# Kernel tuning notes

Hardware: AMD Instinct MI355X
Metric: run time of the kernel (lower is better)

The kernel has to match this reference:

```python
import jax, jax.numpy as jnp
import numpy as np

N, E, VD, HD, ES = 10000, 80000, 32, 64, 68
NET_IN = VD * VD + 2 * HD + ES   # 1220: f2s(1024) + s[e0](64) + s[e1](64) + edge_s(68)
SELF_IN = VD * VD + 2 * HD       # 1152: temp_f2s(1024) + s(64) + s_c(64)
OUT_D = VD * VD + HD             # 1088: vector channel mixer + scalar update


def _lecun(k, fin, fout):
    return jax.random.normal(k, (fin, fout), jnp.float32) / jnp.sqrt(jnp.float32(fin))


def setup_inputs() -> dict:
    ks = jax.random.split(jax.random.key(0), 16)
    return {
        "f": jax.random.normal(ks[0], (N, 3, VD), jnp.float32),
        "s": jax.random.normal(ks[1], (N, HD), jnp.float32),
        "edge_f": jax.random.normal(ks[2], (E, 3, 1), jnp.float32),
        "edge_s": jax.random.normal(ks[3], (E, ES), jnp.float32),
        "W_emb1": _lecun(ks[4], 2 * VD + 1, VD),
        "net_W1": _lecun(ks[5], NET_IN, HD), "net_b1": jnp.zeros((HD,), jnp.float32),
        "net_W2": _lecun(ks[6], HD, HD), "net_b2": jnp.zeros((HD,), jnp.float32),
        "net_W3": _lecun(ks[7], HD, OUT_D), "net_b3": jnp.zeros((OUT_D,), jnp.float32),
        "W_emb2": _lecun(ks[8], 2 * VD, VD),
        "self_W1": _lecun(ks[9], SELF_IN, HD), "self_b1": jnp.zeros((HD,), jnp.float32),
        "self_W2": _lecun(ks[10], HD, HD), "self_b2": jnp.zeros((HD,), jnp.float32),
        "self_W3": _lecun(ks[11], HD, OUT_D), "self_b3": jnp.zeros((OUT_D,), jnp.float32),
        "edge_index": jax.random.randint(ks[12], (2, E), 0, N),
    }


def _mlp(x, W1, b1, W2, b2, W3, b3):
    h = jax.nn.relu(x @ W1 + b1)
    h = jax.nn.relu(h @ W2 + b2)
    return h @ W3 + b3


def _segment_mean(x, ids, n):
    tot = jax.ops.segment_sum(x, ids, num_segments=n)
    cnt = jax.ops.segment_sum(jnp.ones(ids.shape, x.dtype), ids, num_segments=n)
    return tot / jnp.maximum(cnt, 1.0).reshape((n,) + (1,) * (x.ndim - 1))


def _forward(f, s, edge_f, edge_s,
             W_emb1, net_W1, net_b1, net_W2, net_b2, net_W3, net_b3,
             W_emb2, self_W1, self_b1, self_W2, self_b2, self_W3, self_b3,
             edge_index):
    n = f.shape[0]
    e0, e1 = edge_index[0], edge_index[1]
    # --- edge message: gather -> embed -> gram einsum -> MLP ---
    _f = jnp.concatenate((f[e0], f[e1], edge_f), axis=-1)          # [E,3,2VD+1]
    _s = jnp.concatenate((s[e0], s[e1], edge_s), axis=-1)          # [E,2HD+ES]
    _f = _f @ W_emb1                                               # [E,3,VD]
    f2s = jnp.einsum('eij,eik->ejk', _f, _f).reshape(-1, VD * VD)  # _f^T @ _f, [E,VD*VD]
    Fn = jnp.linalg.norm(f2s, axis=-1, keepdims=True) + 1.0
    c = _mlp(jnp.concatenate((f2s, _s), axis=-1),
             net_W1, net_b1, net_W2, net_b2, net_W3, net_b3) / Fn  # [E,OUT_D]
    f_c = jnp.einsum('eij,ejk->eik', _f, c[:, :VD * VD].reshape(-1, VD, VD))  # [E,3,VD]
    f_c = _segment_mean(f_c, e0, n)                                # [N,3,VD]
    s_c = _segment_mean(c[:, VD * VD:], e0, n)                     # [N,HD]
    # --- node self-update ---
    tf = jnp.concatenate((f, f_c), axis=-1) @ W_emb2               # [N,3,VD]
    tf2s = jnp.einsum('nij,nik->njk', tf, tf).reshape(n, VD * VD)
    Fn2 = jnp.linalg.norm(tf2s, axis=-1, keepdims=True) + 1.0
    c2 = _mlp(jnp.concatenate((tf2s, s, s_c), axis=-1),
              self_W1, self_b1, self_W2, self_b2, self_W3, self_b3) / Fn2
    f_out = jnp.einsum('nij,njk->nik', tf, c2[:, :VD * VD].reshape(-1, VD, VD)) + f
    s_out = c2[:, VD * VD:] + s
    return f_out, s_out


def reference(f, s, edge_f, edge_s,
              W_emb1, net_W1, net_b1, net_W2, net_b2, net_W3, net_b3,
              W_emb2, self_W1, self_b1, self_W2, self_b2, self_W3, self_b3,
              edge_index):
    return _forward(f, s, edge_f, edge_s,
                    W_emb1, net_W1, net_b1, net_W2, net_b2, net_W3, net_b3,
                    W_emb2, self_W1, self_b1, self_W2, self_b2, self_W3, self_b3,
                    edge_index)
```

## Files before the change

### kernel.cpp

```cpp
#include <hip/hip_runtime.h>
#include <math.h>

#define NN 10000
#define NE 80000
#define SFH 102
#define SFB 98
#define SSB 66
#define STX 72
#define NTRI 528
#define SAE 104
#define SAN 72

typedef __attribute__((ext_vector_type(8))) __bf16 bf16x8;
typedef __attribute__((ext_vector_type(8))) short short8v;
typedef __attribute__((ext_vector_type(4))) float f32x4;
typedef __attribute__((ext_vector_type(4))) unsigned uint4v;

__device__ __forceinline__ ushort f2bf(float x) {
  union { float f; unsigned u; } v; v.f = x;
  unsigned r = v.u + 0x7FFFu + ((v.u >> 16) & 1u);
  return (ushort)(r >> 16);
}
__device__ __forceinline__ float bfu(ushort u) {
  union { unsigned x; float f; } v; v.x = (unsigned)u << 16;
  return v.f;
}
__device__ __forceinline__ void tri_ab(int k, int& a, int& b) {
  int aa = 0, rem = k;
  while (rem >= 32 - aa) { rem -= 32 - aa; ++aa; }
  a = aa; b = aa + rem;
}

__global__ __launch_bounds__(1024)
void sgnn_scan(const int* __restrict__ deg, int* __restrict__ cursor,
               int* __restrict__ start) {
  __shared__ int sm[1024];
  __shared__ int carry;
  const int t = threadIdx.x;
  if (t == 0) carry = 0;
  __syncthreads();
  for (int base = 0; base < NN; base += 1024) {
    const int i = base + t;
    const int v = (i < NN) ? deg[i] : 0;
    sm[t] = v;
    __syncthreads();
    #pragma unroll
    for (int d = 1; d < 1024; d <<= 1) {
      const int add = (t >= d) ? sm[t - d] : 0;
      __syncthreads();
      sm[t] += add;
      __syncthreads();
    }
    const int excl = carry + sm[t] - v;
    if (i < NN) { cursor[i] = excl; start[i] = excl; }
    __syncthreads();
    if (t == 1023) carry += sm[1023];
    __syncthreads();
  }
}

__global__ __launch_bounds__(256)
void sgnn_scatter(const int* __restrict__ eidx, int* __restrict__ cursor,
                  int* __restrict__ sorted) {
  const int e = blockIdx.x * 256 + threadIdx.x;
  if (e < NE) {
    const int p = atomicAdd(cursor + eidx[e], 1);
    sorted[p] = e;
  }
}

__global__ __launch_bounds__(256)
void sgnn_wconv(const float* __restrict__ nW1, const float* __restrict__ nW2,
                const float* __restrict__ nW3, const float* __restrict__ sW1,
                const float* __restrict__ sW2, const float* __restrict__ sW3,
                const float* __restrict__ Wemb1, const float* __restrict__ Wemb2,
                const int* __restrict__ eidx, int* __restrict__ deg,
                ushort* __restrict__ wout, ushort* __restrict__ tab) {
  const int gid = blockIdx.x * 256 + threadIdx.x;
  if (gid < NE) atomicAdd(deg + eidx[gid], 1);
  if (gid >= 61 * 4096) {
    const int k = gid - 61 * 4096;
    if (k < NTRI) {
      int a, b; tri_ab(k, a, b);
      tab[k] = (ushort)(a | (b << 8) | ((a != b) ? 0x8000 : 0));
    }
    return;
  }
  const int tile = gid >> 12, idx = gid & 4095;
  const int c = idx >> 6, k = idx & 63;
  float v = 0.f;
  if (tile < 12) {
    const int T = tile;
    if (T < 8 || (T == 8 && k < 16)) {
      const int ktri = T * 64 + k;
      if (ktri < NTRI) {
        int a, b; tri_ab(ktri, a, b);
        v = nW1[(a * 32 + b) * 64 + c];
        if (a != b) v += nW1[(b * 32 + a) * 64 + c];
      }
    } else if (T == 8) { if (k < 20) v = nW1[(1216 + (k - 16)) * 64 + c]; }
    else if (T == 9)   v = nW1[(1024 + k) * 64 + c];
    else if (T == 10)  v = nW1[(1088 + k) * 64 + c];
    else               v = nW1[(1152 + k) * 64 + c];
  } else if (tile == 12) v = nW2[k * 64 + c];
  else if (tile < 30)    v = nW3[k * 1088 + (tile - 13) * 64 + c];
  else if (tile < 41) {
    const int T = tile - 30;
    if (T < 8 || (T == 8 && k < 16)) {
      const int ktri = T * 64 + k;
      if (ktri < NTRI) {
        int a, b; tri_ab(ktri, a, b);
        v = sW1[(a * 32 + b) * 64 + c];
        if (a != b) v += sW1[(b * 32 + a) * 64 + c];
      }
    } else if (T == 9) v = sW1[(1024 + k) * 64 + c];
    else if (T == 10)  v = sW1[(1088 + k) * 64 + c];
  } else if (tile == 41) v = sW2[k * 64 + c];
  else if (tile < 59)    v = sW3[k * 1088 + (tile - 42) * 64 + c];
  else if (tile == 59) {
    const int col = idx / 96, kk = idx % 96;
    v = (col < 32 && kk < 65) ? Wemb1[kk * 32 + col] : 0.f;
  } else {
    const int col = idx >> 6;
    v = (col < 32) ? Wemb2[k * 32 + col] : 0.f;
  }
  wout[gid] = f2bf(v);
}

#define STAGE_W(srcbase) do { const ushort* _s = (srcbase);                      \
  _Pragma("unroll") for (int rr = 0; rr < 2; ++rr) {                             \
    const int idx_ = t + 256 * rr; const int c_ = idx_ >> 3, ko_ = idx_ & 7;     \
    *(short8v*)&Wl[c_ * STX + ko_ * 8] = *(const short8v*)&_s[c_ * 64 + ko_ * 8];\
  } } while (0)

#define WPRE_LOAD(srcbase) do { const ushort* _s = (srcbase);                    \
  wpre0 = *(const short8v*)&_s[(t >> 3) * 64 + (t & 7) * 8];                     \
  wpre1 = *(const short8v*)&_s[(32 + (t >> 3)) * 64 + (t & 7) * 8]; } while (0)

#define WPRE_STORE() do {                                                        \
  *(short8v*)&Wl[(t >> 3) * STX + (t & 7) * 8] = wpre0;                          \
  *(short8v*)&Wl[(32 + (t >> 3)) * STX + (t & 7) * 8] = wpre1; } while (0)

#define MFMA_K64() do {                                                          \
  _Pragma("unroll") for (int kb = 0; kb < 2; ++kb) {                             \
    const bf16x8 af_ = *(const bf16x8*)&Xl[(w * 16 + ll) * STX + kb * 32 + lh * 8]; \
    acc[0] = __builtin_amdgcn_mfma_f32_16x16x32_bf16(af_,                        \
        *(const bf16x8*)&Wl[(     ll) * STX + kb * 32 + lh * 8], acc[0], 0, 0, 0); \
    acc[1] = __builtin_amdgcn_mfma_f32_16x16x32_bf16(af_,                        \
        *(const bf16x8*)&Wl[(16 + ll) * STX + kb * 32 + lh * 8], acc[1], 0, 0, 0); \
    acc[2] = __builtin_amdgcn_mfma_f32_16x16x32_bf16(af_,                        \
        *(const bf16x8*)&Wl[(32 + ll) * STX + kb * 32 + lh * 8], acc[2], 0, 0, 0); \
    acc[3] = __builtin_amdgcn_mfma_f32_16x16x32_bf16(af_,                        \
        *(const bf16x8*)&Wl[(48 + ll) * STX + kb * 32 + lh * 8], acc[3], 0, 0, 0); \
  } } while (0)

#define ZERO_ACC() do { _Pragma("unroll") for (int q = 0; q < 4; ++q)            \
    acc[q] = (f32x4){0.f, 0.f, 0.f, 0.f}; } while (0)

#define PACK_STORE16(dstp) do {                                                  \
  unsigned pk[8];                                                                \
  _Pragma("unroll") for (int q = 0; q < 8; ++q)                                  \
    pk[q] = (unsigned)f2bf(xv[2 * q]) | ((unsigned)f2bf(xv[2 * q + 1]) << 16);   \
  *(uint4v*)(dstp)       = (uint4v){pk[0], pk[1], pk[2], pk[3]};                 \
  *(uint4v*)((dstp) + 8) = (uint4v){pk[4], pk[5], pk[6], pk[7]};                 \
} while (0)

#define TRI16(kt) do {                                                           \
  int prev_a = -1; float fa0 = 0.f, fa1 = 0.f, fa2 = 0.f;                        \
  _Pragma("unroll") for (int m = 0; m < 16; ++m) {                               \
    const int tb = tabL[(kt) + m];                                               \
    const int a_ = tb & 31, b_ = (tb >> 8) & 31;                                 \
    if (a_ != prev_a) { fa0 = bfu(fr[a_]); fa1 = bfu(fr[32 + a_]);               \
                        fa2 = bfu(fr[64 + a_]); prev_a = a_; }                   \
    const float v = fmaf(fa0, bfu(fr[b_]),                                       \
        fmaf(fa1, bfu(fr[32 + b_]), fa2 * bfu(fr[64 + b_])));                    \
    const float wsel = (tb & 0x8000) ? 2.f : 1.f;                                \
    sumsq = fmaf(v * wsel, v, sumsq);                                            \
    xv[m] = v;                                                                   \
  } } while (0)

#define XV_LOAD16(p) do { const float* _p = (p);                                 \
  _Pragma("unroll") for (int q = 0; q < 4; ++q) {                                \
    const float4 v4 = *(const float4*)(_p + 4 * q);                              \
    xv[4 * q + 0] = v4.x; xv[4 * q + 1] = v4.y;                                  \
    xv[4 * q + 2] = v4.z; xv[4 * q + 3] = v4.w; } } while (0)

#define CONSUME_NT() do {                                                        \
  _Pragma("unroll") for (int r = 0; r < 4; ++r) {                                \
    const int row_ = w * 16 + lh * 4 + r;                                        \
    const unsigned u0 = *(const unsigned*)&smFh[row_ * SFH +      nt * 2];       \
    const unsigned u1 = *(const unsigned*)&smFh[row_ * SFH + 32 + nt * 2];       \
    const unsigned u2 = *(const unsigned*)&smFh[row_ * SFH + 64 + nt * 2];       \
    union { unsigned x; float f; } l0, h0, l1, h1, l2, h2;                       \
    l0.x = u0 << 16; h0.x = u0 & 0xffff0000u;                                    \
    l1.x = u1 << 16; h1.x = u1 & 0xffff0000u;                                    \
    l2.x = u2 << 16; h2.x = u2 & 0xffff0000u;                                    \
    _Pragma("unroll") for (int nc = 0; nc < 4; ++nc) {                           \
      const float cv = (acc[nc][r] + b3v[nc]) * ifnr[r];                         \
      const int p = nc & 1;                                                      \
      const float f0 = (nc < 2) ? l0.f : h0.f;                                   \
      const float f1 = (nc < 2) ? l1.f : h1.f;                                   \
      const float f2 = (nc < 2) ? l2.f : h2.f;                                   \
      fch[(r * 3 + 0) * 2 + p] = fmaf(f0, cv, fch[(r * 3 + 0) * 2 + p]);         \
      fch[(r * 3 + 1) * 2 + p] = fmaf(f1, cv, fch[(r * 3 + 1) * 2 + p]);         \
      fch[(r * 3 + 2) * 2 + p] = fmaf(f2, cv, fch[(r * 3 + 2) * 2 + p]);         \
    }                                                                            \
  } } while (0)

#define STAGE_FS() do {                                                          \
  _Pragma("unroll") for (int r = 0; r < 4; ++r) {                                \
    const int row_ = w * 16 + lh * 4 + r;                                        \
    _Pragma("unroll") for (int i = 0; i < 3; ++i) {                              \
      F[row_ * SFB + i * 32 + ll]      = f2bf(fch[(r * 3 + i) * 2 + 0]);         \
      F[row_ * SFB + i * 32 + ll + 16] = f2bf(fch[(r * 3 + i) * 2 + 1]);         \
    }                                                                            \
    _Pragma("unroll") for (int nc = 0; nc < 4; ++nc)                             \
      S[row_ * SSB + nc * 16 + ll] = f2bf(cs[nc * 4 + r]);                       \
  } } while (0)

#define LDS_BYTES 34656

__global__ __launch_bounds__(256, 2)
void sgnn_edge(const float* __restrict__ f, const float* __restrict__ s,
               const float* __restrict__ edge_f, const float* __restrict__ edge_s,
               const float* __restrict__ b1, const float* __restrict__ b2,
               const float* __restrict__ b3,
               const ushort* __restrict__ wbf, const ushort* __restrict__ tab_g,
               const int* __restrict__ eidx, const int* __restrict__ sorted,
               const int* __restrict__ start_g, const int* __restrict__ deg_g,
               float* __restrict__ fc_sum, float* __restrict__ sc_sum) {
  __shared__ __align__(16) char sbuf[LDS_BYTES];
  ushort* smFh = (ushort*)sbuf;
  ushort* F    = (ushort*)sbuf;
  ushort* Xl   = (ushort*)(sbuf + 13056);
  ushort* S    = (ushort*)(sbuf + 13056);
  ushort* Aemb = (ushort*)(sbuf + 13056);
  ushort* Wl   = (ushort*)(sbuf + 22272);
  float*  red  = (float*)(sbuf + 31488);
  int*    snode = (int*)(sbuf + 31488);
  int*    srow0 = snode + 8;
  int*    srow1 = snode + 16;
  int*    sst   = snode + 24;
  int*    sdg   = snode + 32;
  ushort* tabL = (ushort*)(sbuf + 33088);
  float*  iFn  = (float*)(sbuf + 33088);
  int*    es_s = (int*)(sbuf + 34144);
  ushort* e0s  = (ushort*)(sbuf + 34400);
  ushort* e1s  = (ushort*)(sbuf + 34528);

  const int t = threadIdx.x, j = t & 63, w = t >> 6, eb = w * 16;
  const int lh = j >> 4, ll = j & 15;
  const int bid = blockIdx.x;
  const ushort* wembT = wbf + 59 * 4096;
  short8v wpre0, wpre1;

  if (t < 64) {
    const int e = sorted[bid * 64 + t];
    es_s[t] = e;
    e0s[t] = (ushort)eidx[e];
    e1s[t] = (ushort)eidx[NE + e];
  }
  for (int idx = t; idx < NTRI; idx += 256) tabL[idx] = tab_g[idx];
  __syncthreads();

  int str = 0, dgr = 0;
  if (j < 16) {
    const int n_ = e0s[eb + j];
    str = start_g[n_];
    dgr = deg_g[n_];
  }
  WPRE_LOAD(wbf + 0);

  #pragma unroll 1
  for (int h = 0; h < 2; ++h) {
    const int hb = h * 32;
    #pragma unroll 1
    for (int cc = t; cc < 576; cc += 256) {
      const int row = cc / 6, seg = cc - row * 6;
      const int lel = (row * 43) >> 7, il = row - lel * 3;
      const int k0 = seg * 16;
      float xv[16];
      if (seg < 4) {
        const int nd = (seg < 2) ? (int)e0s[hb + lel] : (int)e1s[hb + lel];
        XV_LOAD16(f + nd * 96 + il * 32 + (seg & 1) * 16);
      } else if (seg == 4) {
        xv[0] = edge_f[es_s[hb + lel] * 3 + il];
        #pragma unroll
        for (int m = 1; m < 16; ++m) xv[m] = 0.f;
      } else {
        #pragma unroll
        for (int m = 0; m < 16; ++m) xv[m] = 0.f;
      }
      PACK_STORE16(&Aemb[row * SAE + k0]);
    }
    __syncthreads();
    #pragma unroll 1
    for (int job = w * 3; job < w * 3 + 3; ++job) {
      const int mt = job >> 1, nt = job & 1;
      f32x4 ac = (f32x4){0.f, 0.f, 0.f, 0.f};
      #pragma unroll
      for (int kb = 0; kb < 3; ++kb) {
        const bf16x8 av = *(const bf16x8*)&Aemb[(mt * 16 + ll) * SAE + kb * 32 + lh * 8];
        const bf16x8 bv = *(const bf16x8*)&wembT[(nt * 16 + ll) * 96 + kb * 32 + lh * 8];
        ac = __builtin_amdgcn_mfma_f32_16x16x32_bf16(av, bv, ac, 0, 0, 0);
      }
      #pragma unroll
      for (int r = 0; r < 4; ++r) {
        const int rr = mt * 16 + lh * 4 + r;
        const int lel = (rr * 43) >> 7, il = rr - lel * 3;
        smFh[(hb + lel) * SFH + il * 32 + nt * 16 + ll] = f2bf(ac[r]);
      }
    }
    __syncthreads();
  }

  f32x4 acc[4];
  ZERO_ACC();
  float sumsq = 0.f;

  #pragma unroll 1
  for (int T = 0; T < 12; ++T) {
    __syncthreads();
    WPRE_STORE();
    {
      const ushort* fr = smFh + j * SFH;
      float xv[16];
      if (T < 8) {
        TRI16(T * 64 + w * 16);
      } else if (T == 8) {
        if (w == 0) {
          TRI16(512);
        } else if (w == 1) {
          const float4 v4 = *(const float4*)(edge_s + es_s[j] * 68 + 64);
          xv[0] = v4.x; xv[1] = v4.y; xv[2] = v4.z; xv[3] = v4.w;
          #pragma unroll
          for (int m = 4; m < 16; ++m) xv[m] = 0.f;
        } else {
          #pragma unroll
          for (int m = 0; m < 16; ++m) xv[m] = 0.f;
        }
      } else if (T == 9)  { XV_LOAD16(s + e0s[j] * 64 + w * 16); }
      else if (T == 10)   { XV_LOAD16(s + e1s[j] * 64 + w * 16); }
      else                { XV_LOAD16(edge_s + es_s[j] * 68 + w * 16); }
      PACK_STORE16(&Xl[j * STX + w * 16]);
    }
    __syncthreads();
    WPRE_LOAD(wbf + (T + 1) * 4096);
    MFMA_K64();
  }

  __syncthreads();
  red[w * 64 + j] = sumsq;
  #pragma unroll
  for (int nc = 0; nc < 4; ++nc) {
    const float bv = b1[nc * 16 + ll];
    #pragma unroll
    for (int r = 0; r < 4; ++r)
      Xl[(w * 16 + lh * 4 + r) * STX + nc * 16 + ll] = f2bf(fmaxf(acc[nc][r] + bv, 0.f));
  }
  WPRE_STORE();
  ZERO_ACC();
  __syncthreads();
  if (t < 64) {
    const float ss = red[t] + red[64 + t] + red[128 + t] + red[192 + t];
    iFn[t] = 1.f / (sqrtf(ss) + 1.f);
  }

  MFMA_K64();
  #pragma unroll
  for (int nc = 0; nc < 4; ++nc) {
    const float bv = b2[nc * 16 + ll];
    #pragma unroll
    for (int r = 0; r < 4; ++r)
      Xl[(w * 16 + lh * 4 + r) * STX + nc * 16 + ll] = f2bf(fmaxf(acc[nc][r] + bv, 0.f));
  }

  float fch[24];
  #pragma unroll
  for (int q = 0; q < 24; ++q) fch[q] = 0.f;
  float cs[16];
  float ifnr[4];

  #pragma unroll 1
  for (int nt = 0; nt < 17; ++nt) {
    __syncthreads();
    STAGE_W(wbf + (13 + nt) * 4096);
    float b3v[4];
    #pragma unroll
    for (int nc = 0; nc < 4; ++nc) b3v[nc] = b3[nt * 64 + nc * 16 + ll];
    __syncthreads();
    if (nt == 0) {
      #pragma unroll
      for (int r = 0; r < 4; ++r) ifnr[r] = iFn[w * 16 + lh * 4 + r];
    }
    ZERO_ACC();
    MFMA_K64();
    if (nt < 16) {
      CONSUME_NT();
    } else {
      #pragma unroll
      for (int nc = 0; nc < 4; ++nc)
        #pragma unroll
        for (int r = 0; r < 4; ++r)
          cs[nc * 4 + r] = (acc[nc][r] + b3v[nc]) * ifnr[r];
    }
  }

  __syncthreads();
  STAGE_FS();
  if (t < 8) snode[t] = -1;
  __syncthreads();

  {
    float r0 = 0.f, r1 = 0.f, rs = 0.f;
    int runlen = 0;
    const int gwb = bid * 64 + eb;
    #pragma unroll 1
    for (int m = 0; m < 16; ++m) {
      const int row = eb + m;
      r0 += bfu(F[row * SFB + j]);
      if (j < 32) r1 += bfu(F[row * SFB + 64 + j]);
      rs += bfu(S[row * SSB + j]);
      ++runlen;
      const int n = e0s[row];
      if (m == 15 || e0s[row + 1] != n) {
        const int st = __shfl(str, m);
        const int dg = __shfl(dgr, m);
        const int g1v = gwb + m, g0v = g1v - runlen + 1;
        if (g0v == st && runlen == dg) {
          fc_sum[n * 96 + j] = r0;
          if (j < 32) fc_sum[n * 96 + 64 + j] = r1;
          sc_sum[n * 64 + j] = rs;
        } else {
          const int slot = (g0v == gwb) ? 2 * w : 2 * w + 1;
          if (j == 0) {
            snode[slot] = n; srow0[slot] = row - runlen + 1; srow1[slot] = row;
            sst[slot] = st; sdg[slot] = dg;
          }
        }
        r0 = r1 = rs = 0.f; runlen = 0;
      }
    }
  }
  __syncthreads();

  if (t < 160) {
    const int ch = t;
    int prevn = -1;
    #pragma unroll 1
    for (int ss = 0; ss < 8; ++ss) {
      const int n = snode[ss];
      if (n < 0) continue;
      if (n != prevn) {
        float v = 0.f;
        #pragma unroll 1
        for (int k2 = ss; k2 < 8; ++k2) {
          if (snode[k2] == n) {
            #pragma unroll 1
            for (int row = srow0[k2]; row <= srow1[k2]; ++row)
              v += (ch < 96) ? bfu(F[row * SFB + ch]) : bfu(S[row * SSB + (ch - 96)]);
          } else if (k2 > ss && snode[k2] >= 0) break;
        }
        const bool cib = (sst[ss] >= bid * 64) && (sst[ss] + sdg[ss] <= bid * 64 + 64);
        float* dst = (ch < 96) ? (fc_sum + n * 96 + ch) : (sc_sum + n * 64 + (ch - 96));
        if (cib) *dst = v; else atomicAdd(dst, v);
      }
      prevn = n;
    }
  }
}

__global__ __launch_bounds__(256, 2)
void sgnn_node(const float* __restrict__ f, const float* __restrict__ s,
               const float* __restrict__ b1, const float* __restrict__ b2,
               const float* __restrict__ b3,
               const ushort* __restrict__ wbf, const ushort* __restrict__ tab_g,
               const float* __restrict__ fcm, const float* __restrict__ scm,
               const int* __restrict__ deg_g,
               float* __restrict__ of, float* __restrict__ os) {
  __shared__ __align__(16) char sbuf[LDS_BYTES];
  ushort* smFh = (ushort*)sbuf;
  ushort* F    = (ushort*)sbuf;
  ushort* Xl   = (ushort*)(sbuf + 13056);
  ushort* S    = (ushort*)(sbuf + 13056);
  ushort* Aemb = (ushort*)(sbuf + 13056);
  ushort* Wl   = (ushort*)(sbuf + 22272);
  float*  red  = (float*)(sbuf + 31488);
  float*  icntL = (float*)(sbuf + 31488);
  ushort* tabL = (ushort*)(sbuf + 33088);
  float*  iFn  = (float*)(sbuf + 33088);

  const int t = threadIdx.x, j = t & 63, w = t >> 6, eb = w * 16;
  const int lh = j >> 4, ll = j & 15;
  const int nbase = blockIdx.x * 64;
  const ushort* wembTn = wbf + 60 * 4096;
  short8v wpre0, wpre1;

  for (int idx = t; idx < NTRI; idx += 256) tabL[idx] = tab_g[idx];
  if (t < 64)
    icntL[t] = 1.f / fmaxf((float)deg_g[min(nbase + t, NN - 1)], 1.f);
  WPRE_LOAD(wbf + 30 * 4096);
  __syncthreads();

  #pragma unroll 1
  for (int h = 0; h < 2; ++h) {
    const int hb = h * 32;
    #pragma unroll 1
    for (int cc = t; cc < 384; cc += 256) {
      const int row = cc >> 2, seg = cc & 3;
      const int lel = (row * 43) >> 7, il = row - lel * 3;
      const int nc = min(nbase + hb + lel, NN - 1);
      const int k0 = seg * 16;
      float xv[16];
      if (seg < 2) {
        XV_LOAD16(f + nc * 96 + il * 32 + seg * 16);
      } else {
        XV_LOAD16(fcm + nc * 96 + il * 32 + (seg - 2) * 16);
        const float ic = icntL[hb + lel];
        #pragma unroll
        for (int m = 0; m < 16; ++m) xv[m] *= ic;
      }
      PACK_STORE16(&Aemb[row * SAN + k0]);
    }
    __syncthreads();
    #pragma unroll 1
    for (int job = w * 3; job < w * 3 + 3; ++job) {
      const int mt = job >> 1, nt = job & 1;
      f32x4 ac = (f32x4){0.f, 0.f, 0.f, 0.f};
      #pragma unroll
      for (int kb = 0; kb < 2; ++kb) {
        const bf16x8 av = *(const bf16x8*)&Aemb[(mt * 16 + ll) * SAN + kb * 32 + lh * 8];
        const bf16x8 bv = *(const bf16x8*)&wembTn[(nt * 16 + ll) * 64 + kb * 32 + lh * 8];
        ac = __builtin_amdgcn_mfma_f32_16x16x32_bf16(av, bv, ac, 0, 0, 0);
      }
      #pragma unroll
      for (int r = 0; r < 4; ++r) {
        const int rr = mt * 16 + lh * 4 + r;
        const int lel = (rr * 43) >> 7, il = rr - lel * 3;
        smFh[(hb + lel) * SFH + il * 32 + nt * 16 + ll] = f2bf(ac[r]);
      }
    }
    __syncthreads();
  }

  f32x4 acc[4];
  ZERO_ACC();
  float sumsq = 0.f;

  #pragma unroll 1
  for (int T = 0; T < 11; ++T) {
    __syncthreads();
    WPRE_STORE();
    {
      const ushort* fr = smFh + j * SFH;
      float xv[16];
      if (T < 8) {
        TRI16(T * 64 + w * 16);
      } else if (T == 8) {
        if (w == 0) {
          TRI16(512);
        } else {
          #pragma unroll
          for (int m = 0; m < 16; ++m) xv[m] = 0.f;
        }
      } else if (T == 9) {
        XV_LOAD16(s + min(nbase + j, NN - 1) * 64 + w * 16);
      } else {
        XV_LOAD16(scm + min(nbase + j, NN - 1) * 64 + w * 16);
        const float ic = icntL[j];
        #pragma unroll
        for (int m = 0; m < 16; ++m) xv[m] *= ic;
      }
      PACK_STORE16(&Xl[j * STX + w * 16]);
    }
    __syncthreads();
    WPRE_LOAD(wbf + (31 + T) * 4096);
    MFMA_K64();
  }

  __syncthreads();
  red[w * 64 + j] = sumsq;
  #pragma unroll
  for (int nc = 0; nc < 4; ++nc) {
    const float bv = b1[nc * 16 + ll];
    #pragma unroll
    for (int r = 0; r < 4; ++r)
      Xl[(w * 16 + lh * 4 + r) * STX + nc * 16 + ll] = f2bf(fmaxf(acc[nc][r] + bv, 0.f));
  }
  WPRE_STORE();
  ZERO_ACC();
  __syncthreads();
  if (t < 64) {
    const float ss = red[t] + red[64 + t] + red[128 + t] + red[192 + t];
    iFn[t] = 1.f / (sqrtf(ss) + 1.f);
  }

  MFMA_K64();
  #pragma unroll
  for (int nc = 0; nc < 4; ++nc) {
    const float bv = b2[nc * 16 + ll];
    #pragma unroll
    for (int r = 0; r < 4; ++r)
      Xl[(w * 16 + lh * 4 + r) * STX + nc * 16 + ll] = f2bf(fmaxf(acc[nc][r] + bv, 0.f));
  }

  float fch[24];
  #pragma unroll
  for (int q = 0; q < 24; ++q) fch[q] = 0.f;
  float cs[16];
  float ifnr[4];

  #pragma unroll 1
  for (int nt = 0; nt < 17; ++nt) {
    __syncthreads();
    STAGE_W(wbf + (42 + nt) * 4096);
    float b3v[4];
    #pragma unroll
    for (int nc = 0; nc < 4; ++nc) b3v[nc] = b3[nt * 64 + nc * 16 + ll];
    __syncthreads();
    if (nt == 0) {
      #pragma unroll
      for (int r = 0; r < 4; ++r) ifnr[r] = iFn[w * 16 + lh * 4 + r];
    }
    ZERO_ACC();
    MFMA_K64();
    if (nt < 16) {
      CONSUME_NT();
    } else {
      #pragma unroll
      for (int nc = 0; nc < 4; ++nc)
        #pragma unroll
        for (int r = 0; r < 4; ++r)
          cs[nc * 4 + r] = (acc[nc][r] + b3v[nc]) * ifnr[r];
    }
  }

  __syncthreads();
  STAGE_FS();
  __syncthreads();

  #pragma unroll 1
  for (int m = 0; m < 16; ++m) {
    const int row = eb + m;
    const int n_m = nbase + row;
    if (n_m < NN) {
      of[n_m * 96 + j] = bfu(F[row * SFB + j]) + f[n_m * 96 + j];
      if (j < 32)
        of[n_m * 96 + 64 + j] = bfu(F[row * SFB + 64 + j]) + f[n_m * 96 + 64 + j];
      os[n_m * 64 + j] = bfu(S[row * SSB + j]) + s[n_m * 64 + j];
    }
  }
}

extern "C" void kernel_launch(void* const* d_in, const int* in_sizes, int n_in,
                              void* d_out, int out_size, void* d_ws, size_t ws_size,
                              hipStream_t stream) {
  const float* f      = (const float*)d_in[0];
  const float* s      = (const float*)d_in[1];
  const float* edge_f = (const float*)d_in[2];
  const float* edge_s = (const float*)d_in[3];
  const float* Wemb1  = (const float*)d_in[4];
  const float* nW1 = (const float*)d_in[5];
  const float* nb1 = (const float*)d_in[6];
  const float* nW2 = (const float*)d_in[7];
  const float* nb2 = (const float*)d_in[8];
  const float* nW3 = (const float*)d_in[9];
  const float* nb3 = (const float*)d_in[10];
  const float* Wemb2 = (const float*)d_in[11];
  const float* sW1 = (const float*)d_in[12];
  const float* sb1 = (const float*)d_in[13];
  const float* sW2 = (const float*)d_in[14];
  const float* sb2 = (const float*)d_in[15];
  const float* sW3 = (const float*)d_in[16];
  const float* sb3 = (const float*)d_in[17];
  const int* eidx  = (const int*)d_in[18];

  float* of = (float*)d_out;
  float* os = of + (size_t)NN * 96;

  int* deg    = (int*)d_ws;
  int* cursor = deg + NN;
  int* start  = cursor + NN;
  int* sorted = start + NN;
  ushort* wbf = (ushort*)(sorted + NE);
  ushort* tab = wbf + 61 * 4096;

  hipMemsetAsync(deg, 0, (size_t)NN * 4, stream);
  hipMemsetAsync(d_out, 0, (size_t)NN * 160 * 4, stream);

  hipLaunchKernelGGL(sgnn_wconv, dim3((61 * 4096 + NTRI + 255) / 256), dim3(256),
                     0, stream, nW1, nW2, nW3, sW1, sW2, sW3, Wemb1, Wemb2,
                     eidx, deg, wbf, tab);
  hipLaunchKernelGGL(sgnn_scan, dim3(1), dim3(1024), 0, stream, deg, cursor, start);
  hipLaunchKernelGGL(sgnn_scatter, dim3((NE + 255) / 256), dim3(256), 0, stream,
                     eidx, cursor, sorted);
  hipLaunchKernelGGL(sgnn_edge, dim3(NE / 64), dim3(256), 0, stream,
                     f, s, edge_f, edge_s, nb1, nb2, nb3,
                     wbf, tab, eidx, sorted, start, deg,
                     of , os );
  hipLaunchKernelGGL(sgnn_node, dim3((NN + 63) / 64), dim3(256), 0, stream,
                     f, s, sb1, sb2, sb3,
                     wbf, tab, of , os , deg, of, os);
}
```

Before: 213.2 us.

## Double-buffer X and W LDS tiles to overlap staging with MFMA

Adds a second LDS buffer for both the activation tile and the weight tile in the edge and node kernels. The next K-tile's features are built and its weights stored while the current tile's MFMAs run, so each loop step needs one barrier instead of two. The W3 loop also switches from synchronous staging to register-prefetched, double-buffered weights. LDS per block grows from about 34.6KB to 52.5KB, which may limit how many blocks fit per CU at the requested two blocks.

Result: slower. 236.2 us (+10.8%).

```diff
diff --git a/kernel.cpp b/kernel.cpp
--- a/kernel.cpp
+++ b/kernel.cpp
@@ -127,31 +127,25 @@
   wout[gid] = f2bf(v);
 }
 
-#define STAGE_W(srcbase) do { const ushort* _s = (srcbase);                      \
-  _Pragma("unroll") for (int rr = 0; rr < 2; ++rr) {                             \
-    const int idx_ = t + 256 * rr; const int c_ = idx_ >> 3, ko_ = idx_ & 7;     \
-    *(short8v*)&Wl[c_ * STX + ko_ * 8] = *(const short8v*)&_s[c_ * 64 + ko_ * 8];\
-  } } while (0)
-
 #define WPRE_LOAD(srcbase) do { const ushort* _s = (srcbase);                    \
   wpre0 = *(const short8v*)&_s[(t >> 3) * 64 + (t & 7) * 8];                     \
   wpre1 = *(const short8v*)&_s[(32 + (t >> 3)) * 64 + (t & 7) * 8]; } while (0)
 
-#define WPRE_STORE() do {                                                        \
-  *(short8v*)&Wl[(t >> 3) * STX + (t & 7) * 8] = wpre0;                          \
-  *(short8v*)&Wl[(32 + (t >> 3)) * STX + (t & 7) * 8] = wpre1; } while (0)
-
-#define MFMA_K64() do {                                                          \
+#define WPRE_STORE_TO(Wd) do { ushort* _d = (Wd);                                \
+  *(short8v*)&_d[(t >> 3) * STX + (t & 7) * 8] = wpre0;                          \
+  *(short8v*)&_d[(32 + (t >> 3)) * STX + (t & 7) * 8] = wpre1; } while (0)
+
+#define MFMA_K64_B(Xb, Wb) do { const ushort* _x = (Xb); const ushort* _wl = (Wb);\
   _Pragma("unroll") for (int kb = 0; kb < 2; ++kb) {                             \
-    const bf16x8 af_ = *(const bf16x8*)&Xl[(w * 16 + ll) * STX + kb * 32 + lh * 8]; \
+    const bf16x8 af_ = *(const bf16x8*)&_x[(w * 16 + ll) * STX + kb * 32 + lh * 8]; \
     acc[0] = __builtin_amdgcn_mfma_f32_16x16x32_bf16(af_,                        \
-        *(const bf16x8*)&Wl[(     ll) * STX + kb * 32 + lh * 8], acc[0], 0, 0, 0); \
+        *(const bf16x8*)&_wl[(     ll) * STX + kb * 32 + lh * 8], acc[0], 0, 0, 0); \
     acc[1] = __builtin_amdgcn_mfma_f32_16x16x32_bf16(af_,                        \
-        *(const bf16x8*)&Wl[(16 + ll) * STX + kb * 32 + lh * 8], acc[1], 0, 0, 0); \
+        *(const bf16x8*)&_wl[(16 + ll) * STX + kb * 32 + lh * 8], acc[1], 0, 0, 0); \
     acc[2] = __builtin_amdgcn_mfma_f32_16x16x32_bf16(af_,                        \
-        *(const bf16x8*)&Wl[(32 + ll) * STX + kb * 32 + lh * 8], acc[2], 0, 0, 0); \
+        *(const bf16x8*)&_wl[(32 + ll) * STX + kb * 32 + lh * 8], acc[2], 0, 0, 0); \
     acc[3] = __builtin_amdgcn_mfma_f32_16x16x32_bf16(af_,                        \
-        *(const bf16x8*)&Wl[(48 + ll) * STX + kb * 32 + lh * 8], acc[3], 0, 0, 0); \
+        *(const bf16x8*)&_wl[(48 + ll) * STX + kb * 32 + lh * 8], acc[3], 0, 0, 0); \
   } } while (0)
 
 #define ZERO_ACC() do { _Pragma("unroll") for (int q = 0; q < 4; ++q)            \
@@ -218,7 +212,7 @@
       S[row_ * SSB + nc * 16 + ll] = f2bf(cs[nc * 4 + r]);                       \
   } } while (0)
 
-#define LDS_BYTES 34656
+#define LDS_BYTES 52512
 
 __global__ __launch_bounds__(256, 2)
 void sgnn_edge(const float* __restrict__ f, const float* __restrict__ s,
@@ -232,21 +226,23 @@
   __shared__ __align__(16) char sbuf[LDS_BYTES];
   ushort* smFh = (ushort*)sbuf;
   ushort* F    = (ushort*)sbuf;
-  ushort* Xl   = (ushort*)(sbuf + 13056);
+  ushort* Xl0  = (ushort*)(sbuf + 13056);
   ushort* S    = (ushort*)(sbuf + 13056);
   ushort* Aemb = (ushort*)(sbuf + 13056);
-  ushort* Wl   = (ushort*)(sbuf + 22272);
-  float*  red  = (float*)(sbuf + 31488);
-  int*    snode = (int*)(sbuf + 31488);
+  ushort* Xl1  = (ushort*)(sbuf + 22272);
+  ushort* Wl0  = (ushort*)(sbuf + 31488);
+  ushort* Wl1  = (ushort*)(sbuf + 40704);
+  float*  red  = (float*)(sbuf + 49920);
+  int*    snode = (int*)(sbuf + 49920);
   int*    srow0 = snode + 8;
   int*    srow1 = snode + 16;
   int*    sst   = snode + 24;
   int*    sdg   = snode + 32;
-  ushort* tabL = (ushort*)(sbuf + 33088);
-  float*  iFn  = (float*)(sbuf + 33088);
-  int*    es_s = (int*)(sbuf + 34144);
-  ushort* e0s  = (ushort*)(sbuf + 34400);
-  ushort* e1s  = (ushort*)(sbuf + 34528);
+  ushort* tabL = (ushort*)(sbuf + 50944);
+  float*  iFn  = (float*)(sbuf + 50944);
+  int*    es_s = (int*)(sbuf + 52000);
+  ushort* e0s  = (ushort*)(sbuf + 52256);
+  ushort* e1s  = (ushort*)(sbuf + 52384);
 
   const int t = threadIdx.x, j = t & 63, w = t >> 6, eb = w * 16;
   const int lh = j >> 4, ll = j & 15;
@@ -318,47 +314,53 @@
   ZERO_ACC();
   float sumsq = 0.f;
 
+  #define XSTAGE_E(T, Xd) do { ushort* _xd = (Xd);                               \
+    const ushort* fr = smFh + j * SFH;                                           \
+    float xv[16];                                                                \
+    if ((T) < 8) { TRI16((T) * 64 + w * 16); }                                   \
+    else if ((T) == 8) {                                                         \
+      if (w == 0) { TRI16(512); }                                                \
+      else if (w == 1) {                                                         \
+        const float4 v4 = *(const float4*)(edge_s + es_s[j] * 68 + 64);          \
+        xv[0] = v4.x; xv[1] = v4.y; xv[2] = v4.z; xv[3] = v4.w;                  \
+        _Pragma("unroll") for (int m = 4; m < 16; ++m) xv[m] = 0.f;              \
+      } else { _Pragma("unroll") for (int m = 0; m < 16; ++m) xv[m] = 0.f; }     \
+    }                                                                            \
+    else if ((T) == 9)  { XV_LOAD16(s + e0s[j] * 64 + w * 16); }                 \
+    else if ((T) == 10) { XV_LOAD16(s + e1s[j] * 64 + w * 16); }                 \
+    else                { XV_LOAD16(edge_s + es_s[j] * 68 + w * 16); }           \
+    PACK_STORE16(&_xd[j * STX + w * 16]);                                        \
+  } while (0)
+
+  XSTAGE_E(0, Xl0);
+  WPRE_STORE_TO(Wl0);
+  WPRE_LOAD(wbf + 1 * 4096);
+  __syncthreads();
   #pragma unroll 1
   for (int T = 0; T < 12; ++T) {
-    __syncthreads();
-    WPRE_STORE();
-    {
-      const ushort* fr = smFh + j * SFH;
-      float xv[16];
-      if (T < 8) {
-        TRI16(T * 64 + w * 16);
-      } else if (T == 8) {
-        if (w == 0) {
-          TRI16(512);
-        } else if (w == 1) {
-          const float4 v4 = *(const float4*)(edge_s + es_s[j] * 68 + 64);
-          xv[0] = v4.x; xv[1] = v4.y; xv[2] = v4.z; xv[3] = v4.w;
-          #pragma unroll
-          for (int m = 4; m < 16; ++m) xv[m] = 0.f;
-        } else {
-          #pragma unroll
-          for (int m = 0; m < 16; ++m) xv[m] = 0.f;
-        }
-      } else if (T == 9)  { XV_LOAD16(s + e0s[j] * 64 + w * 16); }
-      else if (T == 10)   { XV_LOAD16(s + e1s[j] * 64 + w * 16); }
-      else                { XV_LOAD16(edge_s + es_s[j] * 68 + w * 16); }
-      PACK_STORE16(&Xl[j * STX + w * 16]);
-    }
-    __syncthreads();
-    WPRE_LOAD(wbf + (T + 1) * 4096);
-    MFMA_K64();
-  }
-
-  __syncthreads();
+    ushort* Xc = (T & 1) ? Xl1 : Xl0;
+    ushort* Wc = (T & 1) ? Wl1 : Wl0;
+    ushort* Xn = (T & 1) ? Xl0 : Xl1;
+    ushort* Wn = (T & 1) ? Wl0 : Wl1;
+    if (T < 11) {
+      XSTAGE_E(T + 1, Xn);
+      WPRE_STORE_TO(Wn);
+      WPRE_LOAD(wbf + (T + 2) * 4096);
+    }
+    MFMA_K64_B(Xc, Wc);
+    __syncthreads();
+  }
+
   red[w * 64 + j] = sumsq;
   #pragma unroll
   for (int nc = 0; nc < 4; ++nc) {
     const float bv = b1[nc * 16 + ll];
     #pragma unroll
     for (int r = 0; r < 4; ++r)
-      Xl[(w * 16 + lh * 4 + r) * STX + nc * 16 + ll] = f2bf(fmaxf(acc[nc][r] + bv, 0.f));
-  }
-  WPRE_STORE();
+      Xl0[(w * 16 + lh * 4 + r) * STX + nc * 16 + ll] = f2bf(fmaxf(acc[nc][r] + bv, 0.f));
+  }
+  WPRE_STORE_TO(Wl0);
+  WPRE_LOAD(wbf + 13 * 4096);
   ZERO_ACC();
   __syncthreads();
   if (t < 64) {
@@ -366,35 +368,39 @@
     iFn[t] = 1.f / (sqrtf(ss) + 1.f);
   }
 
-  MFMA_K64();
+  MFMA_K64_B(Xl0, Wl0);
   #pragma unroll
   for (int nc = 0; nc < 4; ++nc) {
     const float bv = b2[nc * 16 + ll];
     #pragma unroll
     for (int r = 0; r < 4; ++r)
-      Xl[(w * 16 + lh * 4 + r) * STX + nc * 16 + ll] = f2bf(fmaxf(acc[nc][r] + bv, 0.f));
-  }
+      Xl0[(w * 16 + lh * 4 + r) * STX + nc * 16 + ll] = f2bf(fmaxf(acc[nc][r] + bv, 0.f));
+  }
+  WPRE_STORE_TO(Wl1);
+  WPRE_LOAD(wbf + 14 * 4096);
+  __syncthreads();
 
   float fch[24];
   #pragma unroll
   for (int q = 0; q < 24; ++q) fch[q] = 0.f;
   float cs[16];
   float ifnr[4];
+  #pragma unroll
+  for (int r = 0; r < 4; ++r) ifnr[r] = iFn[w * 16 + lh * 4 + r];
 
   #pragma unroll 1
   for (int nt = 0; nt < 17; ++nt) {
-    __syncthreads();
-    STAGE_W(wbf + (13 + nt) * 4096);
+    ushort* Wc = (nt & 1) ? Wl0 : Wl1;
+    ushort* Wn = (nt & 1) ? Wl1 : Wl0;
+    if (nt < 16) {
+      WPRE_STORE_TO(Wn);
+      if (nt < 15) WPRE_LOAD(wbf + (15 + nt) * 4096);
+    }
     float b3v[4];
     #pragma unroll
     for (int nc = 0; nc < 4; ++nc) b3v[nc] = b3[nt * 64 + nc * 16 + ll];
-    __syncthreads();
-    if (nt == 0) {
-      #pragma unroll
-      for (int r = 0; r < 4; ++r) ifnr[r] = iFn[w * 16 + lh * 4 + r];
-    }
     ZERO_ACC();
-    MFMA_K64();
+    MFMA_K64_B(Xl0, Wc);
     if (nt < 16) {
       CONSUME_NT();
     } else {
@@ -404,9 +410,9 @@
         for (int r = 0; r < 4; ++r)
           cs[nc * 4 + r] = (acc[nc][r] + b3v[nc]) * ifnr[r];
     }
-  }
-
-  __syncthreads();
+    __syncthreads();
+  }
+
   STAGE_FS();
   if (t < 8) snode[t] = -1;
   __syncthreads();
@@ -481,14 +487,16 @@
   __shared__ __align__(16) char sbuf[LDS_BYTES];
   ushort* smFh = (ushort*)sbuf;
   ushort* F    = (ushort*)sbuf;
-  ushort* Xl   = (ushort*)(sbuf + 13056);
+  ushort* Xl0  = (ushort*)(sbuf + 13056);
   ushort* S    = (ushort*)(sbuf + 13056);
   ushort* Aemb = (ushort*)(sbuf + 13056);
-  ushort* Wl   = (ushort*)(sbuf + 22272);
-  float*  red  = (float*)(sbuf + 31488);
-  float*  icntL = (float*)(sbuf + 31488);
-  ushort* tabL = (ushort*)(sbuf + 33088);
-  float*  iFn  = (float*)(sbuf + 33088);
+  ushort* Xl1  = (ushort*)(sbuf + 22272);
+  ushort* Wl0  = (ushort*)(sbuf + 31488);
+  ushort* Wl1  = (ushort*)(sbuf + 40704);
+  float*  red  = (float*)(sbuf + 49920);
+  float*  icntL = (float*)(sbuf + 49920);
+  ushort* tabL = (ushort*)(sbuf + 50944);
+  float*  iFn  = (float*)(sbuf + 50944);
 
   const int t = threadIdx.x, j = t & 63, w = t >> 6, eb = w * 16;
   const int lh = j >> 4, ll = j & 15;
@@ -547,47 +555,52 @@
   ZERO_ACC();
   float sumsq = 0.f;
 
+  #define XSTAGE_N(T, Xd) do { ushort* _xd = (Xd);                               \
+    const ushort* fr = smFh + j * SFH;                                           \
+    float xv[16];                                                                \
+    if ((T) < 8) { TRI16((T) * 64 + w * 16); }                                   \
+    else if ((T) == 8) {                                                         \
+      if (w == 0) { TRI16(512); }                                                \
+      else { _Pragma("unroll") for (int m = 0; m < 16; ++m) xv[m] = 0.f; }       \
+    }                                                                            \
+    else if ((T) == 9) { XV_LOAD16(s + min(nbase + j, NN - 1) * 64 + w * 16); }  \
+    else {                                                                       \
+      XV_LOAD16(scm + min(nbase + j, NN - 1) * 64 + w * 16);                     \
+      const float ic = icntL[j];                                                 \
+      _Pragma("unroll") for (int m = 0; m < 16; ++m) xv[m] *= ic;                \
+    }                                                                            \
+    PACK_STORE16(&_xd[j * STX + w * 16]);                                        \
+  } while (0)
+
+  XSTAGE_N(0, Xl0);
+  WPRE_STORE_TO(Wl0);
+  WPRE_LOAD(wbf + 31 * 4096);
+  __syncthreads();
   #pragma unroll 1
   for (int T = 0; T < 11; ++T) {
-    __syncthreads();
-    WPRE_STORE();
-    {
-      const ushort* fr = smFh + j * SFH;
-      float xv[16];
-      if (T < 8) {
-        TRI16(T * 64 + w * 16);
-      } else if (T == 8) {
-        if (w == 0) {
-          TRI16(512);
-        } else {
-          #pragma unroll
-          for (int m = 0; m < 16; ++m) xv[m] = 0.f;
-        }
-      } else if (T == 9) {
-        XV_LOAD16(s + min(nbase + j, NN - 1) * 64 + w * 16);
-      } else {
-        XV_LOAD16(scm + min(nbase + j, NN - 1) * 64 + w * 16);
-        const float ic = icntL[j];
-        #pragma unroll
-        for (int m = 0; m < 16; ++m) xv[m] *= ic;
-      }
-      PACK_STORE16(&Xl[j * STX + w * 16]);
-    }
-    __syncthreads();
-    WPRE_LOAD(wbf + (31 + T) * 4096);
-    MFMA_K64();
-  }
-
-  __syncthreads();
+    ushort* Xc = (T & 1) ? Xl1 : Xl0;
+    ushort* Wc = (T & 1) ? Wl1 : Wl0;
+    ushort* Xn = (T & 1) ? Xl0 : Xl1;
+    ushort* Wn = (T & 1) ? Wl0 : Wl1;
+    if (T < 10) {
+      XSTAGE_N(T + 1, Xn);
+      WPRE_STORE_TO(Wn);
+      WPRE_LOAD(wbf + (32 + T) * 4096);
+    }
+    MFMA_K64_B(Xc, Wc);
+    __syncthreads();
+  }
+
   red[w * 64 + j] = sumsq;
   #pragma unroll
   for (int nc = 0; nc < 4; ++nc) {
     const float bv = b1[nc * 16 + ll];
     #pragma unroll
     for (int r = 0; r < 4; ++r)
-      Xl[(w * 16 + lh * 4 + r) * STX + nc * 16 + ll] = f2bf(fmaxf(acc[nc][r] + bv, 0.f));
-  }
-  WPRE_STORE();
+      Xl0[(w * 16 + lh * 4 + r) * STX + nc * 16 + ll] = f2bf(fmaxf(acc[nc][r] + bv, 0.f));
+  }
+  WPRE_STORE_TO(Wl0);
+  WPRE_LOAD(wbf + 42 * 4096);
   ZERO_ACC();
   __syncthreads();
   if (t < 64) {
@@ -595,35 +608,39 @@
     iFn[t] = 1.f / (sqrtf(ss) + 1.f);
   }
 
-  MFMA_K64();
+  MFMA_K64_B(Xl0, Wl0);
   #pragma unroll
   for (int nc = 0; nc < 4; ++nc) {
     const float bv = b2[nc * 16 + ll];
     #pragma unroll
     for (int r = 0; r < 4; ++r)
-      Xl[(w * 16 + lh * 4 + r) * STX + nc * 16 + ll] = f2bf(fmaxf(acc[nc][r] + bv, 0.f));
-  }
+      Xl0[(w * 16 + lh * 4 + r) * STX + nc * 16 + ll] = f2bf(fmaxf(acc[nc][r] + bv, 0.f));
+  }
+  WPRE_STORE_TO(Wl1);
+  WPRE_LOAD(wbf + 43 * 4096);
+  __syncthreads();
 
   float fch[24];
   #pragma unroll
   for (int q = 0; q < 24; ++q) fch[q] = 0.f;
   float cs[16];
   float ifnr[4];
+  #pragma unroll
+  for (int r = 0; r < 4; ++r) ifnr[r] = iFn[w * 16 + lh * 4 + r];
 
   #pragma unroll 1
   for (int nt = 0; nt < 17; ++nt) {
-    __syncthreads();
-    STAGE_W(wbf + (42 + nt) * 4096);
+    ushort* Wc = (nt & 1) ? Wl0 : Wl1;
+    ushort* Wn = (nt & 1) ? Wl1 : Wl0;
+    if (nt < 16) {
+      WPRE_STORE_TO(Wn);
+      if (nt < 15) WPRE_LOAD(wbf + (44 + nt) * 4096);
+    }
     float b3v[4];
     #pragma unroll
     for (int nc = 0; nc < 4; ++nc) b3v[nc] = b3[nt * 64 + nc * 16 + ll];
-    __syncthreads();
-    if (nt == 0) {
-      #pragma unroll
-      for (int r = 0; r < 4; ++r) ifnr[r] = iFn[w * 16 + lh * 4 + r];
-    }
     ZERO_ACC();
-    MFMA_K64();
+    MFMA_K64_B(Xl0, Wc);
     if (nt < 16) {
       CONSUME_NT();
     } else {
@@ -633,9 +650,9 @@
         for (int r = 0; r < 4; ++r)
           cs[nc * 4 + r] = (acc[nc][r] + b3v[nc]) * ifnr[r];
     }
-  }
-
-  __syncthreads();
+    __syncthreads();
+  }
+
   STAGE_FS();
   __syncthreads();
 
```
